# Kernel tuning notes

Hardware: AMD Instinct MI355X
Metric: run time of the kernel (lower is better)

The kernel has to match this reference:

```python
import jax, jax.numpy as jnp
import numpy as np

C = 32  # input multiplicity per irrep (0e and 1o)
D = 32  # output multiplicity per irrep


def pe_inputs(x):
    # x: [B, 2, 3, F]; permutation-equivariant pooled channels
    x_self = x
    x_flavor = x.sum(axis=2, keepdims=True) - x_self
    x_nunubar = x.sum(axis=1, keepdims=True) - x_self
    x_all = x.sum(axis=(1, 2), keepdims=True) - x_self - x_flavor - x_nunubar
    x_flavor = x_flavor / (x.shape[2] - 1)
    x_nunubar = x_nunubar / (x.shape[1] - 1)
    x_all = x_all / ((x.shape[1] - 1) * (x.shape[2] - 1))
    return x_self, x_flavor, x_nunubar, x_all


def _split(x):
    # irreps '32x0e + 32x1o': first C scalars, then C vectors flattened (C,3)
    s = x[..., :C]
    v = x[..., C:].reshape(x.shape[:-1] + (C, 3))
    return s, v


def fctp(x1, x2, W):
    # e3nn FullyConnectedTensorProduct('Cx0e+Cx1o', 'Cx0e+Cx1o', 'Dx0e+Dx1o')
    # W: [4, C, C, D] stacked path weights: [ss->s, vv->s, sv->v, vs->v]
    s1, v1 = _split(x1)
    s2, v2 = _split(x2)
    norm = 1.0 / (C * np.sqrt(2.0))  # sqrt(dim(ir_out) / fan), fan = 2*C^2
    inv_sqrt3 = 1.0 / np.sqrt(3.0)   # wigner_3j(1,1,0) = delta_ij/sqrt(3)
    y_s = norm * (jnp.einsum('uvw,...u,...v->...w', W[0], s1, s2)
                  + inv_sqrt3 * jnp.einsum('uvw,...ui,...vi->...w', W[1], v1, v2))
    y_v = norm * (jnp.einsum('uvw,...u,...vk->...wk', W[2], s1, v2)
                  + jnp.einsum('uvw,...uk,...v->...wk', W[3], v1, s2))
    return jnp.concatenate([y_s, y_v.reshape(y_v.shape[:-2] + (3 * D,))], axis=-1)


def setup_inputs() -> dict:
    key = jax.random.key(0)
    ks = jax.random.split(key, 5)
    B = 16384
    x = jax.random.normal(ks[0], (B, 2, 3, C + 3 * C), dtype=jnp.float32)
    W_self = jax.random.normal(ks[1], (4, C, C, D), dtype=jnp.float32)
    W_flavor = jax.random.normal(ks[2], (4, C, C, D), dtype=jnp.float32)
    W_nunubar = jax.random.normal(ks[3], (4, C, C, D), dtype=jnp.float32)
    W_all = jax.random.normal(ks[4], (4, C, C, D), dtype=jnp.float32)
    return {"x": x, "W_self": W_self, "W_flavor": W_flavor,
            "W_nunubar": W_nunubar, "W_all": W_all}


def reference(x, W_self, W_flavor, W_nunubar, W_all):
    xs, xf, xn, xa = pe_inputs(x)
    y = (fctp(xs, xs, W_self)
         + fctp(xf, xf, W_flavor)
         + fctp(xn, xn, W_nunubar)
         + fctp(xa, xa, W_all))
    return y
```

## Files before the change

### kernel.cpp

```cpp
#include <hip/hip_runtime.h>


typedef _Float16 half8 __attribute__((ext_vector_type(8)));
typedef float   float4_t __attribute__((ext_vector_type(4)));

#define NORM 0.022097086912079608f
#define INV_SQRT3 0.5773502691896258f
#define FS 194

__global__ void prep_kernel(const float* __restrict__ Wa, const float* __restrict__ Wb,
                            const float* __restrict__ Wc, const float* __restrict__ Wd,
                            _Float16* __restrict__ B1s, _Float16* __restrict__ B2s) {
    const float* Ws[4] = {Wa, Wb, Wc, Wd};
    int idx = blockIdx.x * 256 + threadIdx.x;
    if (idx < 262144) {
        int j    = idx & 7;
        int lane = (idx >> 3) & 63;
        int h    = (idx >> 9) & 1;
        int s    = (idx >> 10) & 3;
        int ch   = (idx >> 12) & 15;
        int t    = idx >> 16;
        int m = lane & 15, q = lane >> 4;
        int n = h * 16 + m;
        int k = ch * 128 + s * 32 + q * 8 + j;
        int seg = k >> 10, u = (k >> 5) & 31, v = k & 31;
        const float* W = Ws[t];
        float val;
        if (seg == 0) val = NORM * W[0 * 32768 + u * 1024 + v * 32 + n];
        else          val = NORM * INV_SQRT3 * W[1 * 32768 + u * 1024 + v * 32 + n];
        B1s[idx] = (_Float16)val;
    } else {
        int idx2 = idx - 262144;
        if (idx2 < 131072) {
            int j    = idx2 & 7;
            int lane = (idx2 >> 3) & 63;
            int h    = (idx2 >> 9) & 1;
            int s2   = (idx2 >> 10) & 1;
            int ch   = (idx2 >> 11) & 15;
            int t    = idx2 >> 15;
            int m = lane & 15, q = lane >> 4;
            int n = h * 16 + m;
            int k = ch * 64 + s2 * 32 + q * 8 + j;
            int u = k >> 5, v = k & 31;
            const float* W = Ws[t];
            float val = NORM * (W[2 * 32768 + u * 1024 + v * 32 + n] +
                                W[3 * 32768 + v * 1024 + u * 32 + n]);
            B2s[idx2] = (_Float16)val;
        }
    }
}

__launch_bounds__(256, 2)
__global__ void petp_main(const float* __restrict__ x,
                          const _Float16* __restrict__ B1s,
                          const _Float16* __restrict__ B2s,
                          float* __restrict__ y) {
    __shared__ _Float16 featT[128 * FS];

    const int tid  = threadIdx.x;
    const int wave = tid >> 6;
    const int lane = tid & 63;
    const int m = lane & 15;
    const int q = lane >> 4;
    const int wg = blockIdx.x;
    const int pbase = wave * 48;

    float4_t acc_s[3][2];
    float4_t acc_v[9][2];
    float4_t zero = {0.f, 0.f, 0.f, 0.f};
#pragma unroll
    for (int i = 0; i < 3; ++i) { acc_s[i][0] = zero; acc_s[i][1] = zero; }
#pragma unroll
    for (int i = 0; i < 9; ++i) { acc_v[i][0] = zero; acc_v[i][1] = zero; }

    const float* xg = x + (size_t)wg * (192 * 128);

#pragma unroll 1
    for (int t = 0; t < 4; ++t) {
        __syncthreads();
#pragma unroll 1
        for (int it = 0; it < 16; ++it) {
            int item = it * 256 + tid;
            int b = item >> 7;
            int c = item & 127;
            const float* bp = xg + b * 768 + c;
            float v00 = bp[0],   v01 = bp[128], v02 = bp[256];
            float v10 = bp[384], v11 = bp[512], v12 = bp[640];
            float rs0 = v00 + v01 + v02, rs1 = v10 + v11 + v12;
            float cs0 = v00 + v10, cs1 = v01 + v11, cs2 = v02 + v12;
            float tot = rs0 + rs1;
            float xv[6] = {v00, v01, v02, v10, v11, v12};
            float rs[2] = {rs0, rs1};
            float cs[3] = {cs0, cs1, cs2};
            int row;
            if (c < 32) row = c;
            else { int cc = c - 32; row = 32 + (cc % 3) * 32 + (cc / 3); }
#pragma unroll
            for (int p6 = 0; p6 < 6; ++p6) {
                int i = p6 / 3, j = p6 % 3;
                float xvv = xv[p6];
                float f;
                if      (t == 0) f = xvv;
                else if (t == 1) f = (rs[i] - xvv) * 0.5f;
                else if (t == 2) f = cs[j] - xvv;
                else             f = (tot - rs[i] - cs[j] + xvv) * 0.5f;
                int posL = b * 6 + p6;
                featT[row * FS + posL] = (_Float16)f;
            }
        }
        __syncthreads();

        half8 p_ss[3];
        half8 p_v[3][3];
#pragma unroll
        for (int tl = 0; tl < 3; ++tl) {
            int posL = pbase + tl * 16 + m;
#pragma unroll
            for (int j = 0; j < 8; ++j)
                p_ss[tl][j] = featT[(q * 8 + j) * FS + posL];
#pragma unroll
            for (int i = 0; i < 3; ++i)
#pragma unroll
                for (int j = 0; j < 8; ++j)
                    p_v[tl][i][j] = featT[(32 + i * 32 + q * 8 + j) * FS + posL];
        }

        const _Float16* B1w = B1s + t * 65536 + lane * 8;
        const _Float16* B2w = B2s + t * 32768 + lane * 8;

#pragma unroll 1
        for (int ch = 0; ch < 16; ++ch) {
            half8 b1f[2][4];
            half8 b2f[2][2];
#pragma unroll
            for (int s = 0; s < 4; ++s) {
                b1f[0][s] = *(const half8*)(B1w + ((ch * 4 + s) * 2 + 0) * 512);
                b1f[1][s] = *(const half8*)(B1w + ((ch * 4 + s) * 2 + 1) * 512);
            }
#pragma unroll
            for (int s2 = 0; s2 < 2; ++s2) {
                b2f[0][s2] = *(const half8*)(B2w + ((ch * 2 + s2) * 2 + 0) * 512);
                b2f[1][s2] = *(const half8*)(B2w + ((ch * 2 + s2) * 2 + 1) * 512);
            }

            if (ch < 8) {
#pragma unroll
                for (int s = 0; s < 4; ++s) {
                    int u = ch * 4 + s;
#pragma unroll
                    for (int tl = 0; tl < 3; ++tl) {
                        int posL = pbase + tl * 16 + m;
                        _Float16 bc = featT[u * FS + posL];
                        half8 af = p_ss[tl] * bc;
                        acc_s[tl][0] = __builtin_amdgcn_mfma_f32_16x16x32_f16(af, b1f[0][s], acc_s[tl][0], 0, 0, 0);
                        acc_s[tl][1] = __builtin_amdgcn_mfma_f32_16x16x32_f16(af, b1f[1][s], acc_s[tl][1], 0, 0, 0);
                    }
                }
            } else {
#pragma unroll
                for (int s = 0; s < 4; ++s) {
                    int u = (ch - 8) * 4 + s;
#pragma unroll
                    for (int tl = 0; tl < 3; ++tl) {
                        int posL = pbase + tl * 16 + m;
                        _Float16 g0 = featT[(32 + u) * FS + posL];
                        _Float16 g1 = featT[(64 + u) * FS + posL];
                        _Float16 g2 = featT[(96 + u) * FS + posL];
                        half8 af = p_v[tl][0] * g0 + p_v[tl][1] * g1 + p_v[tl][2] * g2;
                        acc_s[tl][0] = __builtin_amdgcn_mfma_f32_16x16x32_f16(af, b1f[0][s], acc_s[tl][0], 0, 0, 0);
                        acc_s[tl][1] = __builtin_amdgcn_mfma_f32_16x16x32_f16(af, b1f[1][s], acc_s[tl][1], 0, 0, 0);
                    }
                }
            }
#pragma unroll
            for (int s2 = 0; s2 < 2; ++s2) {
                int u = ch * 2 + s2;
                _Float16 bcs[3];
#pragma unroll
                for (int sub = 0; sub < 3; ++sub)
                    bcs[sub] = featT[u * FS + pbase + sub * 16 + m];
#pragma unroll
                for (int tv = 0; tv < 9; ++tv) {
                    int sub = tv % 3, kc = tv / 3;
                    half8 af = p_v[sub][kc] * bcs[sub];
                    acc_v[tv][0] = __builtin_amdgcn_mfma_f32_16x16x32_f16(af, b2f[0][s2], acc_v[tv][0], 0, 0, 0);
                    acc_v[tv][1] = __builtin_amdgcn_mfma_f32_16x16x32_f16(af, b2f[1][s2], acc_v[tv][1], 0, 0, 0);
                }
            }
        }
    }

    float* yg = y + (size_t)wg * (192 * 128);
#pragma unroll
    for (int tl = 0; tl < 3; ++tl) {
#pragma unroll
        for (int nh = 0; nh < 2; ++nh) {
            int w = nh * 16 + m;
#pragma unroll
            for (int r = 0; r < 4; ++r) {
                int pos = wave * 48 + tl * 16 + q * 4 + r;
                yg[pos * 128 + w] = acc_s[tl][nh][r];
            }
        }
    }
#pragma unroll
    for (int tv = 0; tv < 9; ++tv) {
        int sub = tv % 3, kc = tv / 3;
#pragma unroll
        for (int nh = 0; nh < 2; ++nh) {
            int w = nh * 16 + m;
#pragma unroll
            for (int r = 0; r < 4; ++r) {
                int pos = wave * 48 + sub * 16 + q * 4 + r;
                yg[pos * 128 + 32 + 3 * w + kc] = acc_v[tv][nh][r];
            }
        }
    }
}

extern "C" void kernel_launch(void* const* d_in, const int* in_sizes, int n_in,
                              void* d_out, int out_size, void* d_ws, size_t ws_size,
                              hipStream_t stream) {
    const float* x  = (const float*)d_in[0];
    const float* Wa = (const float*)d_in[1];
    const float* Wb = (const float*)d_in[2];
    const float* Wc = (const float*)d_in[3];
    const float* Wd = (const float*)d_in[4];
    float* y = (float*)d_out;

    _Float16* B1s = (_Float16*)d_ws;
    _Float16* B2s = B1s + 262144;

    int nbatch = in_sizes[0] / 768;
    int nwg = nbatch / 32;

    prep_kernel<<<(262144 + 131072) / 256, 256, 0, stream>>>(Wa, Wb, Wc, Wd, B1s, B2s);
    petp_main<<<nwg, 256, 0, stream>>>(x, B1s, B2s, y);
}
```

Baseline: 228.5 us.

## Shrink workgroup tiles to 16 batches with 3 waves and load weights lazily

Each workgroup now handles 16 batch elements (96 positions) with 3 waves of 32 positions each instead of 32 elements with 4 waves of 48. The shared feature buffer halves and per-wave accumulators drop from 12 to 8 tiles. Weight fragments are loaded right before use rather than all at the top of each chunk. The aim is lower register and LDS pressure for higher occupancy and twice as many workgroups. The cost is that B weight fragments are reused across fewer positions, so global/L2 weight traffic per output rises.

After: 241.1 us. 5.5% more time.

```diff
diff --git a/kernel.cpp b/kernel.cpp
--- a/kernel.cpp
+++ b/kernel.cpp
@@ -6,7 +6,7 @@
 
 #define NORM 0.022097086912079608f
 #define INV_SQRT3 0.5773502691896258f
-#define FS 194
+#define FS 98
 
 __global__ void prep_kernel(const float* __restrict__ Wa, const float* __restrict__ Wb,
                             const float* __restrict__ Wc, const float* __restrict__ Wd,
@@ -50,7 +50,7 @@
     }
 }
 
-__launch_bounds__(256, 2)
+__launch_bounds__(192, 3)
 __global__ void petp_main(const float* __restrict__ x,
                           const _Float16* __restrict__ B1s,
                           const _Float16* __restrict__ B2s,
@@ -58,62 +58,64 @@
     __shared__ _Float16 featT[128 * FS];
 
     const int tid  = threadIdx.x;
-    const int wave = tid >> 6;
+    const int wave = tid / 64;
     const int lane = tid & 63;
     const int m = lane & 15;
     const int q = lane >> 4;
     const int wg = blockIdx.x;
-    const int pbase = wave * 48;
-
-    float4_t acc_s[3][2];
-    float4_t acc_v[9][2];
+    const int pbase = wave * 32;
+
+    float4_t acc_s[2][2];
+    float4_t acc_v[6][2];
     float4_t zero = {0.f, 0.f, 0.f, 0.f};
 #pragma unroll
-    for (int i = 0; i < 3; ++i) { acc_s[i][0] = zero; acc_s[i][1] = zero; }
-#pragma unroll
-    for (int i = 0; i < 9; ++i) { acc_v[i][0] = zero; acc_v[i][1] = zero; }
-
-    const float* xg = x + (size_t)wg * (192 * 128);
+    for (int i = 0; i < 2; ++i) { acc_s[i][0] = zero; acc_s[i][1] = zero; }
+#pragma unroll
+    for (int i = 0; i < 6; ++i) { acc_v[i][0] = zero; acc_v[i][1] = zero; }
+
+    const float* xg = x + (size_t)wg * (96 * 128);
 
 #pragma unroll 1
     for (int t = 0; t < 4; ++t) {
         __syncthreads();
 #pragma unroll 1
-        for (int it = 0; it < 16; ++it) {
-            int item = it * 256 + tid;
-            int b = item >> 7;
-            int c = item & 127;
-            const float* bp = xg + b * 768 + c;
-            float v00 = bp[0],   v01 = bp[128], v02 = bp[256];
-            float v10 = bp[384], v11 = bp[512], v12 = bp[640];
-            float rs0 = v00 + v01 + v02, rs1 = v10 + v11 + v12;
-            float cs0 = v00 + v10, cs1 = v01 + v11, cs2 = v02 + v12;
-            float tot = rs0 + rs1;
-            float xv[6] = {v00, v01, v02, v10, v11, v12};
-            float rs[2] = {rs0, rs1};
-            float cs[3] = {cs0, cs1, cs2};
-            int row;
-            if (c < 32) row = c;
-            else { int cc = c - 32; row = 32 + (cc % 3) * 32 + (cc / 3); }
-#pragma unroll
-            for (int p6 = 0; p6 < 6; ++p6) {
-                int i = p6 / 3, j = p6 % 3;
-                float xvv = xv[p6];
-                float f;
-                if      (t == 0) f = xvv;
-                else if (t == 1) f = (rs[i] - xvv) * 0.5f;
-                else if (t == 2) f = cs[j] - xvv;
-                else             f = (tot - rs[i] - cs[j] + xvv) * 0.5f;
-                int posL = b * 6 + p6;
-                featT[row * FS + posL] = (_Float16)f;
+        for (int it = 0; it < 11; ++it) {
+            int item = it * 192 + tid;
+            if (item < 2048) {
+                int b = item >> 7;
+                int c = item & 127;
+                const float* bp = xg + b * 768 + c;
+                float v00 = bp[0],   v01 = bp[128], v02 = bp[256];
+                float v10 = bp[384], v11 = bp[512], v12 = bp[640];
+                float rs0 = v00 + v01 + v02, rs1 = v10 + v11 + v12;
+                float cs0 = v00 + v10, cs1 = v01 + v11, cs2 = v02 + v12;
+                float tot = rs0 + rs1;
+                float xv[6] = {v00, v01, v02, v10, v11, v12};
+                float rs[2] = {rs0, rs1};
+                float cs[3] = {cs0, cs1, cs2};
+                int row;
+                if (c < 32) row = c;
+                else { int cc = c - 32; row = 32 + (cc % 3) * 32 + (cc / 3); }
+#pragma unroll
+                for (int p6 = 0; p6 < 6; ++p6) {
+                    int i = p6 / 3, j = p6 % 3;
+                    float xvv = xv[p6];
+                    float f;
+                    if      (t == 0) f = xvv;
+                    else if (t == 1) f = (rs[i] - xvv) * 0.5f;
+                    else if (t == 2) f = cs[j] - xvv;
+                    else             f = (tot - rs[i] - cs[j] + xvv) * 0.5f;
+                    int posL = b * 6 + p6;
+                    featT[row * FS + posL] = (_Float16)f;
+                }
             }
         }
         __syncthreads();
 
-        half8 p_ss[3];
-        half8 p_v[3][3];
-#pragma unroll
-        for (int tl = 0; tl < 3; ++tl) {
+        half8 p_ss[2];
+        half8 p_v[2][3];
+#pragma unroll
+        for (int tl = 0; tl < 2; ++tl) {
             int posL = pbase + tl * 16 + m;
 #pragma unroll
             for (int j = 0; j < 8; ++j)
@@ -130,88 +132,81 @@
 
 #pragma unroll 1
         for (int ch = 0; ch < 16; ++ch) {
-            half8 b1f[2][4];
-            half8 b2f[2][2];
-#pragma unroll
-            for (int s = 0; s < 4; ++s) {
-                b1f[0][s] = *(const half8*)(B1w + ((ch * 4 + s) * 2 + 0) * 512);
-                b1f[1][s] = *(const half8*)(B1w + ((ch * 4 + s) * 2 + 1) * 512);
-            }
-#pragma unroll
-            for (int s2 = 0; s2 < 2; ++s2) {
-                b2f[0][s2] = *(const half8*)(B2w + ((ch * 2 + s2) * 2 + 0) * 512);
-                b2f[1][s2] = *(const half8*)(B2w + ((ch * 2 + s2) * 2 + 1) * 512);
-            }
-
             if (ch < 8) {
 #pragma unroll
                 for (int s = 0; s < 4; ++s) {
                     int u = ch * 4 + s;
-#pragma unroll
-                    for (int tl = 0; tl < 3; ++tl) {
+                    half8 bf0 = *(const half8*)(B1w + ((ch * 4 + s) * 2 + 0) * 512);
+                    half8 bf1 = *(const half8*)(B1w + ((ch * 4 + s) * 2 + 1) * 512);
+#pragma unroll
+                    for (int tl = 0; tl < 2; ++tl) {
                         int posL = pbase + tl * 16 + m;
                         _Float16 bc = featT[u * FS + posL];
                         half8 af = p_ss[tl] * bc;
-                        acc_s[tl][0] = __builtin_amdgcn_mfma_f32_16x16x32_f16(af, b1f[0][s], acc_s[tl][0], 0, 0, 0);
-                        acc_s[tl][1] = __builtin_amdgcn_mfma_f32_16x16x32_f16(af, b1f[1][s], acc_s[tl][1], 0, 0, 0);
+                        acc_s[tl][0] = __builtin_amdgcn_mfma_f32_16x16x32_f16(af, bf0, acc_s[tl][0], 0, 0, 0);
+                        acc_s[tl][1] = __builtin_amdgcn_mfma_f32_16x16x32_f16(af, bf1, acc_s[tl][1], 0, 0, 0);
                     }
                 }
             } else {
 #pragma unroll
                 for (int s = 0; s < 4; ++s) {
                     int u = (ch - 8) * 4 + s;
-#pragma unroll
-                    for (int tl = 0; tl < 3; ++tl) {
+                    half8 bf0 = *(const half8*)(B1w + ((ch * 4 + s) * 2 + 0) * 512);
+                    half8 bf1 = *(const half8*)(B1w + ((ch * 4 + s) * 2 + 1) * 512);
+#pragma unroll
+                    for (int tl = 0; tl < 2; ++tl) {
                         int posL = pbase + tl * 16 + m;
                         _Float16 g0 = featT[(32 + u) * FS + posL];
                         _Float16 g1 = featT[(64 + u) * FS + posL];
                         _Float16 g2 = featT[(96 + u) * FS + posL];
                         half8 af = p_v[tl][0] * g0 + p_v[tl][1] * g1 + p_v[tl][2] * g2;
-                        acc_s[tl][0] = __builtin_amdgcn_mfma_f32_16x16x32_f16(af, b1f[0][s], acc_s[tl][0], 0, 0, 0);
-                        acc_s[tl][1] = __builtin_amdgcn_mfma_f32_16x16x32_f16(af, b1f[1][s], acc_s[tl][1], 0, 0, 0);
+                        acc_s[tl][0] = __builtin_amdgcn_mfma_f32_16x16x32_f16(af, bf0, acc_s[tl][0], 0, 0, 0);
+                        acc_s[tl][1] = __builtin_amdgcn_mfma_f32_16x16x32_f16(af, bf1, acc_s[tl][1], 0, 0, 0);
                     }
                 }
             }
 #pragma unroll
             for (int s2 = 0; s2 < 2; ++s2) {
                 int u = ch * 2 + s2;
-                _Float16 bcs[3];
-#pragma unroll
-                for (int sub = 0; sub < 3; ++sub)
+                half8 bf0 = *(const half8*)(B2w + ((ch * 2 + s2) * 2 + 0) * 512);
+                half8 bf1 = *(const half8*)(B2w + ((ch * 2 + s2) * 2 + 1) * 512);
+                _Float16 bcs[2];
+#pragma unroll
+                for (int sub = 0; sub < 2; ++sub)
                     bcs[sub] = featT[u * FS + pbase + sub * 16 + m];
 #pragma unroll
-                for (int tv = 0; tv < 9; ++tv) {
-                    int sub = tv % 3, kc = tv / 3;
+                for (int tv = 0; tv < 6; ++tv) {
+                    int sub = tv & 1, kc = tv >> 1;
                     half8 af = p_v[sub][kc] * bcs[sub];
-                    acc_v[tv][0] = __builtin_amdgcn_mfma_f32_16x16x32_f16(af, b2f[0][s2], acc_v[tv][0], 0, 0, 0);
-                    acc_v[tv][1] = __builtin_amdgcn_mfma_f32_16x16x32_f16(af, b2f[1][s2], acc_v[tv][1], 0, 0, 0);
-                }
-            }
-        }
-    }
-
-    float* yg = y + (size_t)wg * (192 * 128);
-#pragma unroll
-    for (int tl = 0; tl < 3; ++tl) {
+                    acc_v[tv][0] = __builtin_amdgcn_mfma_f32_16x16x32_f16(af, bf0, acc_v[tv][0], 0, 0, 0);
+                    acc_v[tv][1] = __builtin_amdgcn_mfma_f32_16x16x32_f16(af, bf1, acc_v[tv][1], 0, 0, 0);
+                }
+            }
+        }
+    }
+
+    float* yg = y + (size_t)wg * (96 * 128);
+#pragma unroll
+    for (int tl = 0; tl < 2; ++tl) {
 #pragma unroll
         for (int nh = 0; nh < 2; ++nh) {
             int w = nh * 16 + m;
 #pragma unroll
             for (int r = 0; r < 4; ++r) {
-                int pos = wave * 48 + tl * 16 + q * 4 + r;
+                int pos = wave * 32 + tl * 16 + q * 4 + r;
                 yg[pos * 128 + w] = acc_s[tl][nh][r];
             }
         }
     }
 #pragma unroll
-    for (int tv = 0; tv < 9; ++tv) {
-        int sub = tv % 3, kc = tv / 3;
+    for (int tv = 0; tv < 6; ++tv) {
+        int sub = tv & 1, kc = tv >> 1;
 #pragma unroll
         for (int nh = 0; nh < 2; ++nh) {
             int w = nh * 16 + m;
 #pragma unroll
             for (int r = 0; r < 4; ++r) {
-                int pos = wave * 48 + sub * 16 + q * 4 + r;
+                int pos = wave * 32 + sub * 16 + q * 4 + r;
                 yg[pos * 128 + 32 + 3 * w + kc] = acc_v[tv][nh][r];
             }
         }
@@ -232,8 +227,8 @@
     _Float16* B2s = B1s + 262144;
 
     int nbatch = in_sizes[0] / 768;
-    int nwg = nbatch / 32;
+    int nwg = nbatch / 16;
 
     prep_kernel<<<(262144 + 131072) / 256, 256, 0, stream>>>(Wa, Wb, Wc, Wd, B1s, B2s);
-    petp_main<<<nwg, 256, 0, stream>>>(x, B1s, B2s, y);
+    petp_main<<<nwg, 192, 0, stream>>>(x, B1s, B2s, y);
 }
```
